# Performance work log

Measured on AMD Instinct MI355X. Metric: run time of the kernel, lower is better.

Reference implementation:

```python
import jax, jax.numpy as jnp
import numpy as np

B, N, M = 256, 512, 1024  # batch, n_vars, max_claims
EPS = 1e-7  # clamp probs to keep logs finite (mirrors torch BCE's -100 log clamp)


def setup_inputs() -> dict:
    key = jax.random.key(0)
    k1, k2, k3, k4, k5, k6 = jax.random.split(key, 6)
    posterior_adjacency = jax.random.uniform(k1, (B, N, N), dtype=jnp.float32)
    var_a = jax.random.randint(k2, (B, M), 0, N, dtype=jnp.int32)
    var_b = jax.random.randint(k3, (B, M), 0, N, dtype=jnp.int32)
    relation_type = jax.random.randint(k4, (B, M), 0, 5, dtype=jnp.int32)
    is_true = jax.random.randint(k5, (B, M), 0, 2, dtype=jnp.int32)
    claim_mask = jax.random.randint(k6, (B, M), 0, 2, dtype=jnp.int32).astype(bool)  # True = padding
    return {
        "posterior_adjacency": posterior_adjacency,
        "var_a": var_a,
        "var_b": var_b,
        "relation_type": relation_type,
        "is_true": is_true,
        "claim_mask": claim_mask,
    }


def reference(posterior_adjacency, var_a, var_b, relation_type, is_true, claim_mask):
    # Batched gather of edge probabilities: p[b, j] = adj[b, var_a[b,j], var_b[b,j]]
    b_idx = jnp.arange(posterior_adjacency.shape[0])[:, None]  # [B, 1]
    p = posterior_adjacency[b_idx, var_a, var_b]               # [B, M]

    # Relation codes: 0=CAUSES, 1=FORBIDS, 2=ANCESTOR, 3=NON_ANCESTOR, else -> 0.5
    flip = (relation_type == 1) | (relation_type == 3)
    prob = jnp.where(flip, 1.0 - p, p)
    prob = jnp.where(relation_type >= 4, 0.5, prob)
    prob = jnp.clip(prob, EPS, 1.0 - EPS)

    t = is_true.astype(prob.dtype)
    per_claim = -(t * jnp.log(prob) + (1.0 - t) * jnp.log1p(-prob))  # BCE on probabilities

    valid = (~claim_mask).astype(prob.dtype)
    n_valid = jnp.sum(valid)
    loss = jnp.where(n_valid > 0,
                     jnp.sum(per_claim * valid) / jnp.maximum(n_valid, 1.0),
                     jnp.array(0.0, dtype=prob.dtype))
    return loss
```

## Files before the change

kernel.cpp:

```cpp
#include <hip/hip_runtime.h>
#include <math.h>

#define BB 256
#define NN 512
#define MM 1024
#define TOTAL (BB * MM)
#define EPS_P 1e-7f


__global__ void detect_mask_kernel(const unsigned char* __restrict__ mask_raw,
                                   int* __restrict__ flag) {
    int f = 0;
    for (int i = 0; i < 1024; ++i) {
        if ((i & 3) != 0 && mask_raw[i] != 0) { f = 1; break; }
    }
    *flag = f;
}

__global__ __launch_bounds__(256)
void claim_loss_kernel(const float* __restrict__ adj,
                       const int*   __restrict__ var_a,
                       const int*   __restrict__ var_b,
                       const int*   __restrict__ rel,
                       const int*   __restrict__ is_true,
                       const void*  __restrict__ mask,
                       const int*   __restrict__ mask_flag,
                       float* __restrict__ loss_sum,
                       int*   __restrict__ valid_cnt) {
    const int j = blockIdx.x * blockDim.x + threadIdx.x;
    const int bytes_mode = *mask_flag;

    float loss  = 0.0f;
    int   valid = 0;
    if (j < TOTAL) {
        int m = bytes_mode ? (int)((const unsigned char*)mask)[j]
                           : ((const int*)mask)[j];
        if (m == 0) {
            const int b = j >> 10;
            const int a = var_a[j];
            const int c = var_b[j];
            const int r = rel[j];
            const int t = is_true[j];
            float p = adj[(size_t)b * (NN * NN) + a * NN + c];
            float prob = (r == 1 || r == 3) ? (1.0f - p) : p;
            if (r >= 4) prob = 0.5f;
            prob = fminf(fmaxf(prob, EPS_P), 1.0f - EPS_P);
            loss = t ? -logf(prob) : -log1pf(-prob);
            valid = 1;
        }
    }

    #pragma unroll
    for (int off = 32; off > 0; off >>= 1) {
        loss  += __shfl_down(loss, off, 64);
        valid += __shfl_down(valid, off, 64);
    }

    __shared__ float s_l[4];
    __shared__ int   s_v[4];
    const int lane = threadIdx.x & 63;
    const int wave = threadIdx.x >> 6;
    if (lane == 0) { s_l[wave] = loss; s_v[wave] = valid; }
    __syncthreads();
    if (threadIdx.x == 0) {
        float L = s_l[0] + s_l[1] + s_l[2] + s_l[3];
        int   V = s_v[0] + s_v[1] + s_v[2] + s_v[3];
        atomicAdd(loss_sum, L);
        atomicAdd(valid_cnt, V);
    }
}

__global__ void finalize_kernel(const float* __restrict__ loss_sum,
                                const int*   __restrict__ valid_cnt,
                                float* __restrict__ out) {
    float n = (float)(*valid_cnt);
    out[0] = (n > 0.0f) ? (*loss_sum / fmaxf(n, 1.0f)) : 0.0f;
}

extern "C" void kernel_launch(void* const* d_in, const int* in_sizes, int n_in,
                              void* d_out, int out_size, void* d_ws, size_t ws_size,
                              hipStream_t stream) {
    const float* adj     = (const float*)d_in[0];
    const int*   var_a   = (const int*)d_in[1];
    const int*   var_b   = (const int*)d_in[2];
    const int*   rel     = (const int*)d_in[3];
    const int*   is_true = (const int*)d_in[4];
    const void*  mask    = d_in[5];

    float* ws_sum  = (float*)d_ws;
    int*   ws_cnt  = (int*)d_ws + 1;
    int*   ws_flag = (int*)d_ws + 2;
    float* out     = (float*)d_out;

    hipMemsetAsync(d_ws, 0, 16, stream);
    detect_mask_kernel<<<1, 1, 0, stream>>>((const unsigned char*)mask, ws_flag);
    claim_loss_kernel<<<TOTAL / 256, 256, 0, stream>>>(
        adj, var_a, var_b, rel, is_true, mask, ws_flag, ws_sum, ws_cnt);
    finalize_kernel<<<1, 1, 0, stream>>>(ws_sum, ws_cnt, out);
}
```

Measured before the change: 382.8 us.

## Inline mask-format detection and replace atomics with two-pass partial reduction

Drops the memset and the serial single-thread mask-detection kernel. Each wavefront now detects the mask format itself with a ballot over the first 64 words. Global atomics are replaced by per-block partial sums written to workspace, which a single 1024-thread kernel then reduces. This cuts launches from four to two and removes atomic contention, at the cost of redundant detection loads in every block.

```diff
diff --git a/kernel.cpp b/kernel.cpp
--- a/kernel.cpp
+++ b/kernel.cpp
@@ -5,49 +5,41 @@
 #define NN 512
 #define MM 1024
 #define TOTAL (BB * MM)
+#define NBLK (TOTAL / 256)
 #define EPS_P 1e-7f
 
 
-__global__ void detect_mask_kernel(const unsigned char* __restrict__ mask_raw,
-                                   int* __restrict__ flag) {
-    int f = 0;
-    for (int i = 0; i < 1024; ++i) {
-        if ((i & 3) != 0 && mask_raw[i] != 0) { f = 1; break; }
-    }
-    *flag = f;
-}
+__global__ __launch_bounds__(256)
+void claim_loss_main(const float* __restrict__ adj,
+                     const int*   __restrict__ var_a,
+                     const int*   __restrict__ var_b,
+                     const int*   __restrict__ rel,
+                     const int*   __restrict__ is_true,
+                     const unsigned int* __restrict__ mask_raw,
+                     float* __restrict__ part_sum,
+                     float* __restrict__ part_cnt) {
+    const unsigned int w = mask_raw[threadIdx.x & 63];
+    const bool bytes_mode = (__ballot((w & 0xFFFFFF00u) != 0u) != 0ull);
 
-__global__ __launch_bounds__(256)
-void claim_loss_kernel(const float* __restrict__ adj,
-                       const int*   __restrict__ var_a,
-                       const int*   __restrict__ var_b,
-                       const int*   __restrict__ rel,
-                       const int*   __restrict__ is_true,
-                       const void*  __restrict__ mask,
-                       const int*   __restrict__ mask_flag,
-                       float* __restrict__ loss_sum,
-                       int*   __restrict__ valid_cnt) {
-    const int j = blockIdx.x * blockDim.x + threadIdx.x;
-    const int bytes_mode = *mask_flag;
+    const int j = blockIdx.x * 256 + threadIdx.x;
+
+    const int m = bytes_mode ? (int)((const unsigned char*)mask_raw)[j]
+                             : ((const int*)mask_raw)[j];
 
     float loss  = 0.0f;
-    int   valid = 0;
-    if (j < TOTAL) {
-        int m = bytes_mode ? (int)((const unsigned char*)mask)[j]
-                           : ((const int*)mask)[j];
-        if (m == 0) {
-            const int b = j >> 10;
-            const int a = var_a[j];
-            const int c = var_b[j];
-            const int r = rel[j];
-            const int t = is_true[j];
-            float p = adj[(size_t)b * (NN * NN) + a * NN + c];
-            float prob = (r == 1 || r == 3) ? (1.0f - p) : p;
-            if (r >= 4) prob = 0.5f;
-            prob = fminf(fmaxf(prob, EPS_P), 1.0f - EPS_P);
-            loss = t ? -logf(prob) : -log1pf(-prob);
-            valid = 1;
-        }
+    float valid = 0.0f;
+    if (m == 0) {
+        const int b = j >> 10;
+        const int a = var_a[j];
+        const int c = var_b[j];
+        const int r = rel[j];
+        const int t = is_true[j];
+        float p = adj[((size_t)b << 18) + (a << 9) + c];
+        float prob = (r == 1 || r == 3) ? (1.0f - p) : p;
+        if (r >= 4) prob = 0.5f;
+        prob = fminf(fmaxf(prob, EPS_P), 1.0f - EPS_P);
+        loss  = t ? -logf(prob) : -log1pf(-prob);
+        valid = 1.0f;
     }
 
     #pragma unroll
@@ -57,24 +49,43 @@
     }
 
     __shared__ float s_l[4];
-    __shared__ int   s_v[4];
+    __shared__ float s_v[4];
     const int lane = threadIdx.x & 63;
     const int wave = threadIdx.x >> 6;
     if (lane == 0) { s_l[wave] = loss; s_v[wave] = valid; }
     __syncthreads();
     if (threadIdx.x == 0) {
-        float L = s_l[0] + s_l[1] + s_l[2] + s_l[3];
-        int   V = s_v[0] + s_v[1] + s_v[2] + s_v[3];
-        atomicAdd(loss_sum, L);
-        atomicAdd(valid_cnt, V);
+        part_sum[blockIdx.x] = s_l[0] + s_l[1] + s_l[2] + s_l[3];
+        part_cnt[blockIdx.x] = s_v[0] + s_v[1] + s_v[2] + s_v[3];
     }
 }
 
-__global__ void finalize_kernel(const float* __restrict__ loss_sum,
-                                const int*   __restrict__ valid_cnt,
-                                float* __restrict__ out) {
-    float n = (float)(*valid_cnt);
-    out[0] = (n > 0.0f) ? (*loss_sum / fmaxf(n, 1.0f)) : 0.0f;
+__global__ __launch_bounds__(1024)
+void claim_loss_final(const float* __restrict__ part_sum,
+                      const float* __restrict__ part_cnt,
+                      float* __restrict__ out) {
+    float s = part_sum[threadIdx.x];
+    float c = part_cnt[threadIdx.x];
+
+    #pragma unroll
+    for (int off = 32; off > 0; off >>= 1) {
+        s += __shfl_down(s, off, 64);
+        c += __shfl_down(c, off, 64);
+    }
+
+    __shared__ float s_l[16];
+    __shared__ float s_v[16];
+    const int lane = threadIdx.x & 63;
+    const int wave = threadIdx.x >> 6;
+    if (lane == 0) { s_l[wave] = s; s_v[wave] = c; }
+    __syncthreads();
+
+    if (threadIdx.x == 0) {
+        float S = 0.0f, C = 0.0f;
+        #pragma unroll
+        for (int i = 0; i < 16; ++i) { S += s_l[i]; C += s_v[i]; }
+        out[0] = (C > 0.0f) ? (S / fmaxf(C, 1.0f)) : 0.0f;
+    }
 }
 
 extern "C" void kernel_launch(void* const* d_in, const int* in_sizes, int n_in,
@@ -85,16 +96,13 @@
     const int*   var_b   = (const int*)d_in[2];
     const int*   rel     = (const int*)d_in[3];
     const int*   is_true = (const int*)d_in[4];
-    const void*  mask    = d_in[5];
+    const unsigned int* mask = (const unsigned int*)d_in[5];
 
-    float* ws_sum  = (float*)d_ws;
-    int*   ws_cnt  = (int*)d_ws + 1;
-    int*   ws_flag = (int*)d_ws + 2;
-    float* out     = (float*)d_out;
+    float* part_sum = (float*)d_ws;
+    float* part_cnt = (float*)d_ws + NBLK;
+    float* out      = (float*)d_out;
 
-    hipMemsetAsync(d_ws, 0, 16, stream);
-    detect_mask_kernel<<<1, 1, 0, stream>>>((const unsigned char*)mask, ws_flag);
-    claim_loss_kernel<<<TOTAL / 256, 256, 0, stream>>>(
-        adj, var_a, var_b, rel, is_true, mask, ws_flag, ws_sum, ws_cnt);
-    finalize_kernel<<<1, 1, 0, stream>>>(ws_sum, ws_cnt, out);
+    claim_loss_main<<<NBLK, 256, 0, stream>>>(
+        adj, var_a, var_b, rel, is_true, mask, part_sum, part_cnt);
+    claim_loss_final<<<1, 1024, 0, stream>>>(part_sum, part_cnt, out);
 }
```

After: 309.1 us. 19.3% less time.
